# Performance work log

Hardware: AMD Instinct MI355X
Metric: run time of the kernel (lower is better)

Reference implementation:

```python
import jax, jax.numpy as jnp
import numpy as np

B, N, D_IN, D_OUT = 4, 2048, 1024, 1024


def setup_inputs() -> dict:
    key = jax.random.key(0)
    k0, k1, k2, k3 = jax.random.split(key, 4)
    x = jax.random.normal(k0, (B, N, D_IN), dtype=jnp.float32)
    # torch Linear weight is [out, in]; store transposed [in, out] for x @ W
    W_query = jax.random.normal(k1, (D_IN, D_OUT), dtype=jnp.float32) * (D_IN ** -0.5)
    W_key = jax.random.normal(k2, (D_IN, D_OUT), dtype=jnp.float32) * (D_IN ** -0.5)
    W_value = jax.random.normal(k3, (D_IN, D_OUT), dtype=jnp.float32) * (D_IN ** -0.5)
    return {"x": x, "W_query": W_query, "W_key": W_key, "W_value": W_value}


def reference(x, W_query, W_key, W_value):
    # x: [B, N, D_IN]
    num_tokens = x.shape[1]
    embed_dim = x.shape[2]  # NB: original scales by INPUT embed dim
    q = jnp.einsum('bnd,de->bne', x, W_query)  # [B, N, D_OUT]
    k = jnp.einsum('bnd,de->bne', x, W_key)
    v = jnp.einsum('bnd,de->bne', x, W_value)
    scores = jnp.einsum('bqe,bke->bqk', q, k)  # [B, N, N]
    idx = jnp.arange(num_tokens)
    causal_mask = idx[None, :] > idx[:, None]  # True above diagonal
    scores = jnp.where(causal_mask[None, :, :], -jnp.inf, scores)
    scale = jnp.asarray(embed_dim, scores.dtype) ** 0.5
    attn = jax.nn.softmax(scores / scale, axis=-1)  # dropout p=0 (eval)
    context = jnp.einsum('bqk,bke->bqe', attn, v)  # [B, N, D_OUT]
    return context
```

## Files before the change

kernel.cpp:

```cpp
#include <hip/hip_runtime.h>


typedef __attribute__((ext_vector_type(8))) _Float16 half8;
typedef __attribute__((ext_vector_type(4))) _Float16 half4v;
typedef __attribute__((ext_vector_type(4))) float floatx4;

#define AS1 __attribute__((address_space(1)))
#define AS3 __attribute__((address_space(3)))

__device__ __forceinline__ void load16_lds(void* lds, const void* g) {
  __builtin_amdgcn_global_load_lds((AS1 void*)g, (AS3 void*)lds, 16, 0, 0);
}


__global__ __launch_bounds__(256)
void conv_f32_f16(const float* __restrict__ in, _Float16* __restrict__ out) {
  const int i = (blockIdx.x * 256 + threadIdx.x) << 2;
  float4 v = *(const float4*)(in + i);
  half4v o = { (_Float16)v.x, (_Float16)v.y, (_Float16)v.z, (_Float16)v.w };
  *(half4v*)(out + i) = o;
}

__global__ __launch_bounds__(256)
void transpose_w(const float* __restrict__ W0, const float* __restrict__ W1,
                 const float* __restrict__ W2, _Float16* __restrict__ Wt) {
  const float* W = blockIdx.z == 0 ? W0 : (blockIdx.z == 1 ? W1 : W2);
  _Float16* out = Wt + (long long)blockIdx.z * 1048576;
  __shared__ _Float16 t[32][33];
  const int tx = threadIdx.x, ty = threadIdx.y;
  const int n0 = blockIdx.x << 5, k0 = blockIdx.y << 5;
#pragma unroll
  for (int i = 0; i < 4; ++i)
    t[ty + i * 8][tx] = (_Float16)W[(long long)(k0 + ty + i * 8) * 1024 + n0 + tx];
  __syncthreads();
#pragma unroll
  for (int i = 0; i < 4; ++i)
    out[(long long)(n0 + ty + i * 8) * 1024 + k0 + tx] = t[tx][ty + i * 8];
}

__global__ __launch_bounds__(256)
void zero_l(float* __restrict__ l) {
  const int i = (blockIdx.x * 256 + threadIdx.x) << 2;
  *(float4*)(l + i) = float4{0.f, 0.f, 0.f, 0.f};
}

__global__ __launch_bounds__(256)
void gemm_qkv(const _Float16* __restrict__ A, const _Float16* __restrict__ B,
              _Float16* __restrict__ Q, _Float16* __restrict__ Kh,
              _Float16* __restrict__ Vt) {
  const int bm = blockIdx.y, bn = blockIdx.x;
  const _Float16* Ab = A + (long long)bm * 128 * 1024;
  const _Float16* Bb = B + (long long)bn * 128 * 1024;

  __shared__ _Float16 As[128][64];
  __shared__ _Float16 Bs[128][64];

  const int tid = threadIdx.x;
  const int wave = tid >> 6, lane = tid & 63;
  const int quad = lane >> 4, lr = lane & 15;
  const int wm = (wave >> 1) << 6, wn = (wave & 1) << 6;
  const int srow = lane >> 3;
  const int goff = ((lane & 7) ^ srow) << 3;

  floatx4 acc[4][4] = {};
  const _Float16* ga = Ab + (long long)(wave * 8 + srow) * 1024 + goff;
  const _Float16* gb = Bb + (long long)(wave * 8 + srow) * 1024 + goff;

  for (int k0 = 0; k0 < 1024; k0 += 64) {
    __syncthreads();
#pragma unroll
    for (int c = 0; c < 4; ++c) {
      load16_lds(&As[wave * 8 + 32 * c][0], ga + c * 32 * 1024);
      load16_lds(&Bs[wave * 8 + 32 * c][0], gb + c * 32 * 1024);
    }
    ga += 64; gb += 64;
    __syncthreads();

#pragma unroll
    for (int kk = 0; kk < 2; ++kk) {
      half8 af[4], bf[4];
#pragma unroll
      for (int i = 0; i < 4; ++i) {
        const int ra = wm + (i << 4) + lr;
        const int rb = wn + (i << 4) + lr;
        af[i] = *(const half8*)&As[ra][(((kk << 2) + quad) ^ (ra & 7)) << 3];
        bf[i] = *(const half8*)&Bs[rb][(((kk << 2) + quad) ^ (rb & 7)) << 3];
      }
#pragma unroll
      for (int i = 0; i < 4; ++i)
#pragma unroll
        for (int j = 0; j < 4; ++j)
          acc[i][j] = __builtin_amdgcn_mfma_f32_16x16x32_f16(af[i], bf[j], acc[i][j], 0, 0, 0);
    }
  }

  const int colb = bn * 128 + wn + lr;
  const int rowb = bm * 128 + wm + (quad << 2);

  if (bn < 16) {
    _Float16* C = (bn < 8) ? Q : Kh;
    const int cb = colb & 1023;
#pragma unroll
    for (int i = 0; i < 4; ++i)
#pragma unroll
      for (int j = 0; j < 4; ++j)
#pragma unroll
        for (int r = 0; r < 4; ++r)
          C[(long long)(rowb + (i << 4) + r) * 1024 + cb + (j << 4)] =
              (_Float16)acc[i][j][r];
  } else {
    const int b = rowb >> 11;
    const int tb = rowb & 2047;
#pragma unroll
    for (int i = 0; i < 4; ++i) {
      const int tok = tb + (i << 4);
#pragma unroll
      for (int j = 0; j < 4; ++j) {
        const int d = (colb & 1023) + (j << 4);
        half4v v = { (_Float16)acc[i][j][0], (_Float16)acc[i][j][1],
                     (_Float16)acc[i][j][2], (_Float16)acc[i][j][3] };
        *(half4v*)&Vt[(long long)b * 2097152 + (long long)d * 2048 + tok] = v;
      }
    }
  }
}

__global__ __launch_bounds__(256)
void gemm_s_exp(const _Float16* __restrict__ Q, const _Float16* __restrict__ Kh,
                _Float16* __restrict__ P, float* __restrict__ l) {
  int t = blockIdx.x;
  const int bz = blockIdx.y;
  int bm = 0;
  for (;;) { const int c = (bm >> 1) + 1; if (t < c) break; t -= c; ++bm; }
  const int bn = t;

  const _Float16* Ab = Q  + (long long)bz * 2097152 + (long long)bm * 64 * 1024;
  const _Float16* Bb = Kh + (long long)bz * 2097152 + (long long)bn * 128 * 1024;

  __shared__ _Float16 As[64][64];
  __shared__ _Float16 Bs[128][64];

  const int tid = threadIdx.x;
  const int wave = tid >> 6, lane = tid & 63;
  const int quad = lane >> 4, lr = lane & 15;
  const int wn = wave << 5;
  const int srow = lane >> 3;
  const int goff = ((lane & 7) ^ srow) << 3;

  floatx4 acc[4][2] = {};
  const _Float16* ga = Ab + (long long)(wave * 8 + srow) * 1024 + goff;
  const _Float16* gb = Bb + (long long)(wave * 8 + srow) * 1024 + goff;

  for (int k0 = 0; k0 < 1024; k0 += 64) {
    __syncthreads();
#pragma unroll
    for (int c = 0; c < 2; ++c)
      load16_lds(&As[wave * 8 + 32 * c][0], ga + c * 32 * 1024);
#pragma unroll
    for (int c = 0; c < 4; ++c)
      load16_lds(&Bs[wave * 8 + 32 * c][0], gb + c * 32 * 1024);
    ga += 64; gb += 64;
    __syncthreads();

#pragma unroll
    for (int kk = 0; kk < 2; ++kk) {
      half8 af[4], bf[2];
#pragma unroll
      for (int i = 0; i < 4; ++i) {
        const int ra = (i << 4) + lr;
        af[i] = *(const half8*)&As[ra][(((kk << 2) + quad) ^ (ra & 7)) << 3];
      }
#pragma unroll
      for (int j = 0; j < 2; ++j) {
        const int rb = wn + (j << 4) + lr;
        bf[j] = *(const half8*)&Bs[rb][(((kk << 2) + quad) ^ (rb & 7)) << 3];
      }
#pragma unroll
      for (int i = 0; i < 4; ++i)
#pragma unroll
        for (int j = 0; j < 2; ++j)
          acc[i][j] = __builtin_amdgcn_mfma_f32_16x16x32_f16(af[i], bf[j], acc[i][j], 0, 0, 0);
    }
  }

  const int colb = bn * 128 + wn + lr;
  const int rowq = bm * 64 + (quad << 2);
  _Float16* Pb = P + (long long)bz * 4194304;
  const float scl = 0.03125f;

  float rs[4][4];
#pragma unroll
  for (int i = 0; i < 4; ++i)
#pragma unroll
    for (int r = 0; r < 4; ++r) rs[i][r] = 0.f;

#pragma unroll
  for (int i = 0; i < 4; ++i)
#pragma unroll
    for (int j = 0; j < 2; ++j)
#pragma unroll
      for (int r = 0; r < 4; ++r) {
        const int q = rowq + (i << 4) + r;
        const int kcol = colb + (j << 4);
        const float p = (kcol <= q) ? __expf(acc[i][j][r] * scl) : 0.f;
        Pb[(long long)q * 2048 + kcol] = (_Float16)p;
        rs[i][r] += p;
      }

#pragma unroll
  for (int i = 0; i < 4; ++i)
#pragma unroll
    for (int r = 0; r < 4; ++r) {
#pragma unroll
      for (int off = 1; off < 16; off <<= 1)
        rs[i][r] += __shfl_xor(rs[i][r], off);
    }
  if (lr == 0) {
    float* lb = l + bz * 2048;
#pragma unroll
    for (int i = 0; i < 4; ++i)
#pragma unroll
      for (int r = 0; r < 4; ++r)
        atomicAdd(&lb[rowq + (i << 4) + r], rs[i][r]);
  }
}

__global__ __launch_bounds__(256)
void gemm_pv(const _Float16* __restrict__ P, const _Float16* __restrict__ Vt,
             const float* __restrict__ l, float* __restrict__ out) {
  const int bn = blockIdx.x, bz = blockIdx.z;
  const int bm = 31 - blockIdx.y;
  const int Keff = 64 * (bm + 1);

  const _Float16* Ab = P  + (long long)bz * 4194304 + (long long)bm * 64 * 2048;
  const _Float16* Bb = Vt + (long long)bz * 2097152 + (long long)bn * 128 * 2048;

  __shared__ _Float16 As[64][64];
  __shared__ _Float16 Bs[128][64];

  const int tid = threadIdx.x;
  const int wave = tid >> 6, lane = tid & 63;
  const int quad = lane >> 4, lr = lane & 15;
  const int wn = wave << 5;
  const int srow = lane >> 3;
  const int goff = ((lane & 7) ^ srow) << 3;

  floatx4 acc[4][2] = {};
  const _Float16* ga = Ab + (long long)(wave * 8 + srow) * 2048 + goff;
  const _Float16* gb = Bb + (long long)(wave * 8 + srow) * 2048 + goff;

  for (int k0 = 0; k0 < Keff; k0 += 64) {
    __syncthreads();
#pragma unroll
    for (int c = 0; c < 2; ++c)
      load16_lds(&As[wave * 8 + 32 * c][0], ga + c * 32 * 2048);
#pragma unroll
    for (int c = 0; c < 4; ++c)
      load16_lds(&Bs[wave * 8 + 32 * c][0], gb + c * 32 * 2048);
    ga += 64; gb += 64;
    __syncthreads();

#pragma unroll
    for (int kk = 0; kk < 2; ++kk) {
      half8 af[4], bf[2];
#pragma unroll
      for (int i = 0; i < 4; ++i) {
        const int ra = (i << 4) + lr;
        af[i] = *(const half8*)&As[ra][(((kk << 2) + quad) ^ (ra & 7)) << 3];
      }
#pragma unroll
      for (int j = 0; j < 2; ++j) {
        const int rb = wn + (j << 4) + lr;
        bf[j] = *(const half8*)&Bs[rb][(((kk << 2) + quad) ^ (rb & 7)) << 3];
      }
#pragma unroll
      for (int i = 0; i < 4; ++i)
#pragma unroll
        for (int j = 0; j < 2; ++j)
          acc[i][j] = __builtin_amdgcn_mfma_f32_16x16x32_f16(af[i], bf[j], acc[i][j], 0, 0, 0);
    }
  }

  const int colb = bn * 128 + wn + lr;
  const int rowq = bm * 64 + (quad << 2);
  const float* lb = l + bz * 2048;
  float* Cb = out + (long long)bz * 2097152;

  float linv[4][4];
#pragma unroll
  for (int i = 0; i < 4; ++i)
#pragma unroll
    for (int r = 0; r < 4; ++r)
      linv[i][r] = 1.0f / lb[rowq + (i << 4) + r];

#pragma unroll
  for (int i = 0; i < 4; ++i)
#pragma unroll
    for (int j = 0; j < 2; ++j)
#pragma unroll
      for (int r = 0; r < 4; ++r)
        Cb[(long long)(rowq + (i << 4) + r) * 1024 + colb + (j << 4)] =
            acc[i][j][r] * linv[i][r];
}


extern "C" void kernel_launch(void* const* d_in, const int* in_sizes, int n_in,
                              void* d_out, int out_size, void* d_ws, size_t ws_size,
                              hipStream_t stream) {
  const float* x  = (const float*)d_in[0];
  const float* Wq = (const float*)d_in[1];
  const float* Wk = (const float*)d_in[2];
  const float* Wv = (const float*)d_in[3];
  float* out = (float*)d_out;

  char* ws = (char*)d_ws;
  _Float16* xh = (_Float16*)(ws);
  _Float16* Wt = (_Float16*)(ws + 16777216);
  _Float16* Q  = (_Float16*)(ws + 23068672);
  _Float16* Kh = (_Float16*)(ws + 39845888);
  _Float16* Vt = (_Float16*)(ws + 56623104);
  _Float16* P  = (_Float16*)(ws + 73400320);
  float*    l  = (float*)   (ws + 106954752);

  conv_f32_f16<<<8192, 256, 0, stream>>>(x, xh);
  transpose_w<<<dim3(32, 32, 3), dim3(32, 8), 0, stream>>>(Wq, Wk, Wv, Wt);
  zero_l<<<8, 256, 0, stream>>>(l);

  gemm_qkv<<<dim3(24, 64), 256, 0, stream>>>(xh, Wt, Q, Kh, Vt);

  gemm_s_exp<<<dim3(272, 4), 256, 0, stream>>>(Q, Kh, P, l);

  gemm_pv<<<dim3(8, 32, 4), 256, 0, stream>>>(P, Vt, l, out);
}
```

Measured before the change: 256.0 us.

## Widen score and PV tiles to 64x256 with causal block skipping, fuse zeroing

The score and PV GEMMs now use 64x256 output tiles, with each wave owning 64 columns, instead of 64x128 tiles. This halves the number of blocks and re-reads of the Q/P rows. In the score kernel, waves whose column sub-tiles lie fully above the causal diagonal skip their K loads, MFMAs and stores. The separate zero_l launch is merged into the conversion kernel as extra blocks. The cost is more accumulators per thread, a larger LDS footprint and fewer blocks to fill the CUs.

```diff
diff --git a/kernel.cpp b/kernel.cpp
--- a/kernel.cpp
+++ b/kernel.cpp
@@ -14,11 +14,17 @@
 
 
 __global__ __launch_bounds__(256)
-void conv_f32_f16(const float* __restrict__ in, _Float16* __restrict__ out) {
-  const int i = (blockIdx.x * 256 + threadIdx.x) << 2;
-  float4 v = *(const float4*)(in + i);
-  half4v o = { (_Float16)v.x, (_Float16)v.y, (_Float16)v.z, (_Float16)v.w };
-  *(half4v*)(out + i) = o;
+void conv_f32_f16(const float* __restrict__ in, _Float16* __restrict__ out,
+                  float* __restrict__ l) {
+  if (blockIdx.x < 8192) {
+    const int i = (blockIdx.x * 256 + threadIdx.x) << 2;
+    float4 v = *(const float4*)(in + i);
+    half4v o = { (_Float16)v.x, (_Float16)v.y, (_Float16)v.z, (_Float16)v.w };
+    *(half4v*)(out + i) = o;
+  } else {
+    const int i = ((blockIdx.x - 8192) * 256 + threadIdx.x) << 2;
+    *(float4*)(l + i) = float4{0.f, 0.f, 0.f, 0.f};
+  }
 }
 
 __global__ __launch_bounds__(256)
@@ -39,12 +45,6 @@
 }
 
 __global__ __launch_bounds__(256)
-void zero_l(float* __restrict__ l) {
-  const int i = (blockIdx.x * 256 + threadIdx.x) << 2;
-  *(float4*)(l + i) = float4{0.f, 0.f, 0.f, 0.f};
-}
-
-__global__ __launch_bounds__(256)
 void gemm_qkv(const _Float16* __restrict__ A, const _Float16* __restrict__ B,
               _Float16* __restrict__ Q, _Float16* __restrict__ Kh,
               _Float16* __restrict__ Vt) {
@@ -131,59 +131,61 @@
   int t = blockIdx.x;
   const int bz = blockIdx.y;
   int bm = 0;
-  for (;;) { const int c = (bm >> 1) + 1; if (t < c) break; t -= c; ++bm; }
+  for (;;) { const int c = (bm >> 2) + 1; if (t < c) break; t -= c; ++bm; }
   const int bn = t;
 
   const _Float16* Ab = Q  + (long long)bz * 2097152 + (long long)bm * 64 * 1024;
-  const _Float16* Bb = Kh + (long long)bz * 2097152 + (long long)bn * 128 * 1024;
+  const _Float16* Bb = Kh + (long long)bz * 2097152 + (long long)bn * 256 * 1024;
+  const int nmaxl = bm * 64 + 63 - bn * 256;
 
   __shared__ _Float16 As[64][64];
-  __shared__ _Float16 Bs[128][64];
+  __shared__ _Float16 Bs[256][64];
 
   const int tid = threadIdx.x;
   const int wave = tid >> 6, lane = tid & 63;
   const int quad = lane >> 4, lr = lane & 15;
-  const int wn = wave << 5;
   const int srow = lane >> 3;
   const int goff = ((lane & 7) ^ srow) << 3;
 
-  floatx4 acc[4][2] = {};
-  const _Float16* ga = Ab + (long long)(wave * 8 + srow) * 1024 + goff;
-  const _Float16* gb = Bb + (long long)(wave * 8 + srow) * 1024 + goff;
+  floatx4 acc[4][4] = {};
+  const _Float16* ga = Ab + (long long)(wave * 16 + srow) * 1024 + goff;
+  const _Float16* gb = Bb + (long long)(wave * 64 + srow) * 1024 + goff;
 
   for (int k0 = 0; k0 < 1024; k0 += 64) {
     __syncthreads();
-#pragma unroll
-    for (int c = 0; c < 2; ++c)
-      load16_lds(&As[wave * 8 + 32 * c][0], ga + c * 32 * 1024);
-#pragma unroll
-    for (int c = 0; c < 4; ++c)
-      load16_lds(&Bs[wave * 8 + 32 * c][0], gb + c * 32 * 1024);
+    load16_lds(&As[wave * 16][0],     ga);
+    load16_lds(&As[wave * 16 + 8][0], ga + 8 * 1024);
+#pragma unroll
+    for (int c = 0; c < 8; ++c)
+      if (wave * 64 + 8 * c <= nmaxl)
+        load16_lds(&Bs[wave * 64 + 8 * c][0], gb + c * 8 * 1024);
     ga += 64; gb += 64;
     __syncthreads();
 
 #pragma unroll
     for (int kk = 0; kk < 2; ++kk) {
-      half8 af[4], bf[2];
+      half8 af[4], bf[4];
 #pragma unroll
       for (int i = 0; i < 4; ++i) {
         const int ra = (i << 4) + lr;
         af[i] = *(const half8*)&As[ra][(((kk << 2) + quad) ^ (ra & 7)) << 3];
       }
 #pragma unroll
-      for (int j = 0; j < 2; ++j) {
-        const int rb = wn + (j << 4) + lr;
-        bf[j] = *(const half8*)&Bs[rb][(((kk << 2) + quad) ^ (rb & 7)) << 3];
-      }
+      for (int j = 0; j < 4; ++j)
+        if (wave * 64 + (j << 4) <= nmaxl) {
+          const int rb = wave * 64 + (j << 4) + lr;
+          bf[j] = *(const half8*)&Bs[rb][(((kk << 2) + quad) ^ (rb & 7)) << 3];
+        }
 #pragma unroll
       for (int i = 0; i < 4; ++i)
 #pragma unroll
-        for (int j = 0; j < 2; ++j)
-          acc[i][j] = __builtin_amdgcn_mfma_f32_16x16x32_f16(af[i], bf[j], acc[i][j], 0, 0, 0);
-    }
-  }
-
-  const int colb = bn * 128 + wn + lr;
+        for (int j = 0; j < 4; ++j)
+          if (wave * 64 + (j << 4) <= nmaxl)
+            acc[i][j] = __builtin_amdgcn_mfma_f32_16x16x32_f16(af[i], bf[j], acc[i][j], 0, 0, 0);
+    }
+  }
+
+  const int n0 = bn * 256 + wave * 64;
   const int rowq = bm * 64 + (quad << 2);
   _Float16* Pb = P + (long long)bz * 4194304;
   const float scl = 0.03125f;
@@ -195,17 +197,19 @@
     for (int r = 0; r < 4; ++r) rs[i][r] = 0.f;
 
 #pragma unroll
-  for (int i = 0; i < 4; ++i)
-#pragma unroll
-    for (int j = 0; j < 2; ++j)
-#pragma unroll
-      for (int r = 0; r < 4; ++r) {
-        const int q = rowq + (i << 4) + r;
-        const int kcol = colb + (j << 4);
-        const float p = (kcol <= q) ? __expf(acc[i][j][r] * scl) : 0.f;
-        Pb[(long long)q * 2048 + kcol] = (_Float16)p;
-        rs[i][r] += p;
-      }
+  for (int j = 0; j < 4; ++j)
+    if (wave * 64 + (j << 4) <= nmaxl) {
+      const int kcol = n0 + (j << 4) + lr;
+#pragma unroll
+      for (int i = 0; i < 4; ++i)
+#pragma unroll
+        for (int r = 0; r < 4; ++r) {
+          const int q = rowq + (i << 4) + r;
+          const float p = (kcol <= q) ? __expf(acc[i][j][r] * scl) : 0.f;
+          Pb[(long long)q * 2048 + kcol] = (_Float16)p;
+          rs[i][r] += p;
+        }
+    }
 
 #pragma unroll
   for (int i = 0; i < 4; ++i)
@@ -233,55 +237,53 @@
   const int Keff = 64 * (bm + 1);
 
   const _Float16* Ab = P  + (long long)bz * 4194304 + (long long)bm * 64 * 2048;
-  const _Float16* Bb = Vt + (long long)bz * 2097152 + (long long)bn * 128 * 2048;
+  const _Float16* Bb = Vt + (long long)bz * 2097152 + (long long)bn * 256 * 2048;
 
   __shared__ _Float16 As[64][64];
-  __shared__ _Float16 Bs[128][64];
+  __shared__ _Float16 Bs[256][64];
 
   const int tid = threadIdx.x;
   const int wave = tid >> 6, lane = tid & 63;
   const int quad = lane >> 4, lr = lane & 15;
-  const int wn = wave << 5;
   const int srow = lane >> 3;
   const int goff = ((lane & 7) ^ srow) << 3;
 
-  floatx4 acc[4][2] = {};
-  const _Float16* ga = Ab + (long long)(wave * 8 + srow) * 2048 + goff;
-  const _Float16* gb = Bb + (long long)(wave * 8 + srow) * 2048 + goff;
+  floatx4 acc[4][4] = {};
+  const _Float16* ga = Ab + (long long)(wave * 16 + srow) * 2048 + goff;
+  const _Float16* gb = Bb + (long long)(wave * 64 + srow) * 2048 + goff;
 
   for (int k0 = 0; k0 < Keff; k0 += 64) {
     __syncthreads();
-#pragma unroll
-    for (int c = 0; c < 2; ++c)
-      load16_lds(&As[wave * 8 + 32 * c][0], ga + c * 32 * 2048);
-#pragma unroll
-    for (int c = 0; c < 4; ++c)
-      load16_lds(&Bs[wave * 8 + 32 * c][0], gb + c * 32 * 2048);
+    load16_lds(&As[wave * 16][0],     ga);
+    load16_lds(&As[wave * 16 + 8][0], ga + 8 * 2048);
+#pragma unroll
+    for (int c = 0; c < 8; ++c)
+      load16_lds(&Bs[wave * 64 + 8 * c][0], gb + c * 8 * 2048);
     ga += 64; gb += 64;
     __syncthreads();
 
 #pragma unroll
     for (int kk = 0; kk < 2; ++kk) {
-      half8 af[4], bf[2];
+      half8 af[4], bf[4];
 #pragma unroll
       for (int i = 0; i < 4; ++i) {
         const int ra = (i << 4) + lr;
         af[i] = *(const half8*)&As[ra][(((kk << 2) + quad) ^ (ra & 7)) << 3];
       }
 #pragma unroll
-      for (int j = 0; j < 2; ++j) {
-        const int rb = wn + (j << 4) + lr;
+      for (int j = 0; j < 4; ++j) {
+        const int rb = wave * 64 + (j << 4) + lr;
         bf[j] = *(const half8*)&Bs[rb][(((kk << 2) + quad) ^ (rb & 7)) << 3];
       }
 #pragma unroll
       for (int i = 0; i < 4; ++i)
 #pragma unroll
-        for (int j = 0; j < 2; ++j)
+        for (int j = 0; j < 4; ++j)
           acc[i][j] = __builtin_amdgcn_mfma_f32_16x16x32_f16(af[i], bf[j], acc[i][j], 0, 0, 0);
     }
   }
 
-  const int colb = bn * 128 + wn + lr;
+  const int d0 = bn * 256 + wave * 64;
   const int rowq = bm * 64 + (quad << 2);
   const float* lb = l + bz * 2048;
   float* Cb = out + (long long)bz * 2097152;
@@ -296,10 +298,10 @@
 #pragma unroll
   for (int i = 0; i < 4; ++i)
 #pragma unroll
-    for (int j = 0; j < 2; ++j)
+    for (int j = 0; j < 4; ++j)
 #pragma unroll
       for (int r = 0; r < 4; ++r)
-        Cb[(long long)(rowq + (i << 4) + r) * 1024 + colb + (j << 4)] =
+        Cb[(long long)(rowq + (i << 4) + r) * 1024 + d0 + (j << 4) + lr] =
             acc[i][j][r] * linv[i][r];
 }
 
@@ -322,13 +324,12 @@
   _Float16* P  = (_Float16*)(ws + 73400320);
   float*    l  = (float*)   (ws + 106954752);
 
-  conv_f32_f16<<<8192, 256, 0, stream>>>(x, xh);
+  conv_f32_f16<<<8200, 256, 0, stream>>>(x, xh, l);
   transpose_w<<<dim3(32, 32, 3), dim3(32, 8), 0, stream>>>(Wq, Wk, Wv, Wt);
-  zero_l<<<8, 256, 0, stream>>>(l);
 
   gemm_qkv<<<dim3(24, 64), 256, 0, stream>>>(xh, Wt, Q, Kh, Vt);
 
-  gemm_s_exp<<<dim3(272, 4), 256, 0, stream>>>(Q, Kh, P, l);
-
-  gemm_pv<<<dim3(8, 32, 4), 256, 0, stream>>>(P, Vt, l, out);
-}
+  gemm_s_exp<<<dim3(144, 4), 256, 0, stream>>>(Q, Kh, P, l);
+
+  gemm_pv<<<dim3(4, 32, 4), 256, 0, stream>>>(P, Vt, l, out);
+}
```

After: 252.0 us. Within noise of the previous version (-1.6%).

## Register-prefetch next K tile in attention GEMMs and fold zeroing into conversion

Applied to the files above, without the earlier changes.

The S and PV GEMM kernels stop using direct global-to-LDS loads. They now prefetch the next K tile into registers while the MFMAs run on the current LDS tile, then write that tile into LDS at the top of the next iteration. The goal is to overlap global load latency with compute, at the cost of extra VGPRs and explicit LDS stores. The separate row-sum zeroing kernel is merged into the fp32-to-fp16 conversion kernel as extra blocks, which removes one launch.

```diff
diff --git a/kernel.cpp b/kernel.cpp
--- a/kernel.cpp
+++ b/kernel.cpp
@@ -14,11 +14,17 @@
 
 
 __global__ __launch_bounds__(256)
-void conv_f32_f16(const float* __restrict__ in, _Float16* __restrict__ out) {
-  const int i = (blockIdx.x * 256 + threadIdx.x) << 2;
-  float4 v = *(const float4*)(in + i);
-  half4v o = { (_Float16)v.x, (_Float16)v.y, (_Float16)v.z, (_Float16)v.w };
-  *(half4v*)(out + i) = o;
+void conv_f32_f16(const float* __restrict__ in, _Float16* __restrict__ out,
+                  float* __restrict__ l) {
+  if (blockIdx.x < 8192) {
+    const int i = (blockIdx.x * 256 + threadIdx.x) << 2;
+    float4 v = *(const float4*)(in + i);
+    half4v o = { (_Float16)v.x, (_Float16)v.y, (_Float16)v.z, (_Float16)v.w };
+    *(half4v*)(out + i) = o;
+  } else {
+    const int i = ((blockIdx.x - 8192) * 256 + threadIdx.x) << 2;
+    *(float4*)(l + i) = float4{0.f, 0.f, 0.f, 0.f};
+  }
 }
 
 __global__ __launch_bounds__(256)
@@ -39,12 +45,6 @@
 }
 
 __global__ __launch_bounds__(256)
-void zero_l(float* __restrict__ l) {
-  const int i = (blockIdx.x * 256 + threadIdx.x) << 2;
-  *(float4*)(l + i) = float4{0.f, 0.f, 0.f, 0.f};
-}
-
-__global__ __launch_bounds__(256)
 void gemm_qkv(const _Float16* __restrict__ A, const _Float16* __restrict__ B,
               _Float16* __restrict__ Q, _Float16* __restrict__ Kh,
               _Float16* __restrict__ Vt) {
@@ -129,10 +129,10 @@
 void gemm_s_exp(const _Float16* __restrict__ Q, const _Float16* __restrict__ Kh,
                 _Float16* __restrict__ P, float* __restrict__ l) {
   int t = blockIdx.x;
-  const int bz = blockIdx.y;
   int bm = 0;
   for (;;) { const int c = (bm >> 1) + 1; if (t < c) break; t -= c; ++bm; }
   const int bn = t;
+  const int bz = blockIdx.y;
 
   const _Float16* Ab = Q  + (long long)bz * 2097152 + (long long)bm * 64 * 1024;
   const _Float16* Bb = Kh + (long long)bz * 2097152 + (long long)bn * 128 * 1024;
@@ -145,22 +145,35 @@
   const int quad = lane >> 4, lr = lane & 15;
   const int wn = wave << 5;
   const int srow = lane >> 3;
-  const int goff = ((lane & 7) ^ srow) << 3;
+  const int schunk = lane & 7;
+  const int goff = (schunk ^ srow) << 3;
 
   floatx4 acc[4][2] = {};
   const _Float16* ga = Ab + (long long)(wave * 8 + srow) * 1024 + goff;
   const _Float16* gb = Bb + (long long)(wave * 8 + srow) * 1024 + goff;
 
-  for (int k0 = 0; k0 < 1024; k0 += 64) {
+  half8 pa[2], pb[4];
+#pragma unroll
+  for (int c = 0; c < 2; ++c) pa[c] = *(const half8*)(ga + c * 32 * 1024);
+#pragma unroll
+  for (int c = 0; c < 4; ++c) pb[c] = *(const half8*)(gb + c * 32 * 1024);
+
+  for (int it = 0; it < 16; ++it) {
     __syncthreads();
 #pragma unroll
     for (int c = 0; c < 2; ++c)
-      load16_lds(&As[wave * 8 + 32 * c][0], ga + c * 32 * 1024);
+      *(half8*)&As[wave * 8 + 32 * c + srow][schunk << 3] = pa[c];
 #pragma unroll
     for (int c = 0; c < 4; ++c)
-      load16_lds(&Bs[wave * 8 + 32 * c][0], gb + c * 32 * 1024);
-    ga += 64; gb += 64;
-    __syncthreads();
+      *(half8*)&Bs[wave * 8 + 32 * c + srow][schunk << 3] = pb[c];
+    __syncthreads();
+    if (it + 1 < 16) {
+      const int k1 = (it + 1) << 6;
+#pragma unroll
+      for (int c = 0; c < 2; ++c) pa[c] = *(const half8*)(ga + c * 32 * 1024 + k1);
+#pragma unroll
+      for (int c = 0; c < 4; ++c) pb[c] = *(const half8*)(gb + c * 32 * 1024 + k1);
+    }
 
 #pragma unroll
     for (int kk = 0; kk < 2; ++kk) {
@@ -202,9 +215,9 @@
       for (int r = 0; r < 4; ++r) {
         const int q = rowq + (i << 4) + r;
         const int kcol = colb + (j << 4);
-        const float p = (kcol <= q) ? __expf(acc[i][j][r] * scl) : 0.f;
-        Pb[(long long)q * 2048 + kcol] = (_Float16)p;
-        rs[i][r] += p;
+        const float pv = (kcol <= q) ? __expf(acc[i][j][r] * scl) : 0.f;
+        Pb[(long long)q * 2048 + kcol] = (_Float16)pv;
+        rs[i][r] += pv;
       }
 
 #pragma unroll
@@ -228,12 +241,13 @@
 __global__ __launch_bounds__(256)
 void gemm_pv(const _Float16* __restrict__ P, const _Float16* __restrict__ Vt,
              const float* __restrict__ l, float* __restrict__ out) {
-  const int bn = blockIdx.x, bz = blockIdx.z;
+  const int dn = blockIdx.x;
   const int bm = 31 - blockIdx.y;
-  const int Keff = 64 * (bm + 1);
+  const int bz = blockIdx.z;
+  const int niter = bm + 1;
 
   const _Float16* Ab = P  + (long long)bz * 4194304 + (long long)bm * 64 * 2048;
-  const _Float16* Bb = Vt + (long long)bz * 2097152 + (long long)bn * 128 * 2048;
+  const _Float16* Bb = Vt + (long long)bz * 2097152 + (long long)dn * 128 * 2048;
 
   __shared__ _Float16 As[64][64];
   __shared__ _Float16 Bs[128][64];
@@ -243,22 +257,37 @@
   const int quad = lane >> 4, lr = lane & 15;
   const int wn = wave << 5;
   const int srow = lane >> 3;
-  const int goff = ((lane & 7) ^ srow) << 3;
+  const int schunk = lane & 7;
+  const int goff = (schunk ^ srow) << 3;
 
   floatx4 acc[4][2] = {};
   const _Float16* ga = Ab + (long long)(wave * 8 + srow) * 2048 + goff;
   const _Float16* gb = Bb + (long long)(wave * 8 + srow) * 2048 + goff;
 
-  for (int k0 = 0; k0 < Keff; k0 += 64) {
+  half8 pa[2], pb[4];
+#pragma unroll
+  for (int c = 0; c < 2; ++c) pa[c] = *(const half8*)(ga + (long long)c * 32 * 2048);
+#pragma unroll
+  for (int c = 0; c < 4; ++c) pb[c] = *(const half8*)(gb + (long long)c * 32 * 2048);
+
+  for (int it = 0; it < niter; ++it) {
     __syncthreads();
 #pragma unroll
     for (int c = 0; c < 2; ++c)
-      load16_lds(&As[wave * 8 + 32 * c][0], ga + c * 32 * 2048);
+      *(half8*)&As[wave * 8 + 32 * c + srow][schunk << 3] = pa[c];
 #pragma unroll
     for (int c = 0; c < 4; ++c)
-      load16_lds(&Bs[wave * 8 + 32 * c][0], gb + c * 32 * 2048);
-    ga += 64; gb += 64;
-    __syncthreads();
+      *(half8*)&Bs[wave * 8 + 32 * c + srow][schunk << 3] = pb[c];
+    __syncthreads();
+    if (it + 1 < niter) {
+      const int k1 = (it + 1) << 6;
+#pragma unroll
+      for (int c = 0; c < 2; ++c)
+        pa[c] = *(const half8*)(ga + (long long)c * 32 * 2048 + k1);
+#pragma unroll
+      for (int c = 0; c < 4; ++c)
+        pb[c] = *(const half8*)(gb + (long long)c * 32 * 2048 + k1);
+    }
 
 #pragma unroll
     for (int kk = 0; kk < 2; ++kk) {
@@ -281,7 +310,7 @@
     }
   }
 
-  const int colb = bn * 128 + wn + lr;
+  const int colb = dn * 128 + wn + lr;
   const int rowq = bm * 64 + (quad << 2);
   const float* lb = l + bz * 2048;
   float* Cb = out + (long long)bz * 2097152;
@@ -322,9 +351,8 @@
   _Float16* P  = (_Float16*)(ws + 73400320);
   float*    l  = (float*)   (ws + 106954752);
 
-  conv_f32_f16<<<8192, 256, 0, stream>>>(x, xh);
+  conv_f32_f16<<<8200, 256, 0, stream>>>(x, xh, l);
   transpose_w<<<dim3(32, 32, 3), dim3(32, 8), 0, stream>>>(Wq, Wk, Wv, Wt);
-  zero_l<<<8, 256, 0, stream>>>(l);
 
   gemm_qkv<<<dim3(24, 64), 256, 0, stream>>>(xh, Wt, Q, Kh, Vt);
 
```

Result: no change. 253.6 us (-0.9%).
